# Kernel optimization log

Hardware: AMD Instinct MI355X
Metric: run time of the kernel (lower is better)

The kernel has to match this reference:

```python
import jax, jax.numpy as jnp
import numpy as np
from jax import lax

C = 128       # capacity
D = 64        # latent_dims
K = 512       # K_vecs
BETA = 0.25
DN = ('NCHW', 'OIHW', 'NCHW')


def conv(x, w, b, stride=2, pad=1):
    y = lax.conv_general_dilated(x, w, (stride, stride), ((pad, pad), (pad, pad)),
                                 dimension_numbers=DN)
    return y + b[None, :, None, None]


def conv_transpose(x, w, b, stride=2, pad=1, k=4):
    # PyTorch ConvTranspose2d weight is (Cin, Cout, kh, kw); emulate via
    # lhs-dilated conv with spatially flipped, IO-swapped kernel.
    w2 = jnp.flip(w, axis=(-2, -1)).transpose(1, 0, 2, 3)  # -> OIHW
    p = k - 1 - pad
    y = lax.conv_general_dilated(x, w2, (1, 1), ((p, p), (p, p)),
                                 lhs_dilation=(stride, stride), dimension_numbers=DN)
    return y + b[None, :, None, None]


def setup_inputs() -> dict:
    key = jax.random.key(0)
    ks = jax.random.split(key, 11)
    s = 0.05
    return {
        'x': jax.random.uniform(ks[0], (32, 1, 256, 256), dtype=jnp.float32),
        'enc_w1': jax.random.normal(ks[1], (C, 1, 4, 4), jnp.float32) * s,
        'enc_b1': jnp.zeros((C,), jnp.float32),
        'enc_w2': jax.random.normal(ks[2], (D, C, 4, 4), jnp.float32) * s,
        'enc_b2': jnp.zeros((D,), jnp.float32),
        'codebook': jax.random.normal(ks[3], (K, D), jnp.float32),
        'dec_w2': jax.random.normal(ks[4], (D, C, 4, 4), jnp.float32) * s,  # ConvT: (Cin,Cout,kh,kw)
        'dec_b2': jnp.zeros((C,), jnp.float32),
        'dec_w1': jax.random.normal(ks[5], (C, 1, 4, 4), jnp.float32) * s,
        'dec_b1': jnp.zeros((1,), jnp.float32),
    }


def reference(x, enc_w1, enc_b1, enc_w2, enc_b2, codebook, dec_w2, dec_b2, dec_w1, dec_b1):
    # ---- encoder ----
    h = jax.nn.relu(conv(x, enc_w1, enc_b1))
    z = jax.nn.relu(conv(h, enc_w2, enc_b2))          # [B, D, H/4, W/4]

    # ---- vector quantizer ----
    z_nhwc = jnp.transpose(z, (0, 2, 3, 1))           # [B, h, w, D]
    flat = z_nhwc.reshape(-1, D)                      # [N, D]
    # mean-over-D squared distance, expanded form (no NxKxD tensor)
    d = (jnp.sum(flat * flat, axis=1, keepdims=True)
         - 2.0 * flat @ codebook.T
         + jnp.sum(codebook * codebook, axis=1)[None, :]) / D   # [N, K]
    idx = jnp.argmin(d, axis=1)                       # [N]
    quantized = codebook[idx].reshape(z_nhwc.shape)   # [B, h, w, D]

    codebook_loss = jnp.mean((quantized - lax.stop_gradient(z_nhwc)) ** 2)
    commitment_loss = jnp.mean((lax.stop_gradient(quantized) - z_nhwc) ** 2)
    vq_loss = codebook_loss + BETA * commitment_loss

    # straight-through estimator (training mode)
    quantized_st = z_nhwc + lax.stop_gradient(quantized - z_nhwc)
    q_nchw = jnp.transpose(quantized_st, (0, 3, 1, 2))

    # ---- decoder ----
    g = jax.nn.relu(conv_transpose(q_nchw, dec_w2, dec_b2))
    x_recon = jax.nn.sigmoid(conv_transpose(g, dec_w1, dec_b1))

    return vq_loss, idx[:, None].astype(jnp.int32), x_recon
```

## Files before the change

kernel.cpp:

```cpp
#include <hip/hip_runtime.h>
#include <math.h>


#define REC_OFF 131073

typedef unsigned short ushort_t;
typedef __attribute__((ext_vector_type(8))) short bf16x8;
typedef __attribute__((ext_vector_type(4))) float f32x4;
typedef __attribute__((ext_vector_type(4))) unsigned int u32x4;
union FragU { u32x4 u; bf16x8 h; };

__device__ __forceinline__ unsigned pack_hilo(float v) {
  unsigned u = __float_as_uint(v);
  unsigned htop = u & 0xFFFF0000u;
  float rf = v - __uint_as_float(htop);
  return htop | (__float_as_uint(rf) >> 16);
}

__global__ __launch_bounds__(64) void zero_loss_k(float* __restrict__ out) {
  if (threadIdx.x == 0) out[0] = 0.f;
}

__global__ __launch_bounds__(256) void repackA2_k(
    const float* __restrict__ ew2,
    ushort_t* __restrict__ hi, ushort_t* __restrict__ lo) {
  int idx = blockIdx.x * 256 + threadIdx.x;
  int j = idx & 7, l = (idx >> 3) & 63, mt = (idx >> 9) & 3, ks = idx >> 11;
  int ci = ((ks >> 2) << 3) + ((l >> 4) << 1) + (j >> 2);
  int ky = ks & 3, kx = j & 3, d = (mt << 4) + (l & 15);
  float val = ew2[((d << 7) + ci) * 16 + (ky << 2) + kx];
  unsigned u = __float_as_uint(val);
  float rf = val - __uint_as_float(u & 0xFFFF0000u);
  hi[idx] = (ushort_t)(u >> 16);
  lo[idx] = (ushort_t)(__float_as_uint(rf) >> 16);
}

__global__ __launch_bounds__(256) void repackA_k(
    const float* __restrict__ dw2,
    ushort_t* __restrict__ hi, ushort_t* __restrict__ lo) {
  int idx = blockIdx.x * 256 + threadIdx.x;
  int j = idx & 7, l = (idx >> 3) & 63, mt = (idx >> 9) & 7;
  int s = (idx >> 12) & 7, v = idx >> 15;
  int co = (mt << 4) + (l & 15);
  int ci = (s << 3) + ((l >> 4) << 1) + (j >> 2);
  int tap = j & 3;
  int Yp = v >> 1, pX = v & 1;
  int kyA = 1 - Yp, kyB = kyA + 2;
  int kxA = pX ? 0 : 1, kxB = kxA + 2;
  int ky = (tap & 2) ? kyB : kyA;
  int kx = (tap & 1) ? kxA : kxB;
  float val = dw2[(((ci << 7) + co) << 4) + (ky << 2) + kx];
  unsigned u = __float_as_uint(val);
  float rf = val - __uint_as_float(u & 0xFFFF0000u);
  hi[idx] = (ushort_t)(u >> 16);
  lo[idx] = (ushort_t)(__float_as_uint(rf) >> 16);
}

__global__ __launch_bounds__(256) void repackCB_k(
    const float* __restrict__ cb,
    ushort_t* __restrict__ hi, ushort_t* __restrict__ lo) {
  int idx = blockIdx.x * 256 + threadIdx.x;
  int j = idx & 7, l = (idx >> 3) & 63, mt = (idx >> 9) & 31, ks = idx >> 14;
  int code = (mt << 4) + (l & 15);
  int k = (ks << 5) + ((l >> 4) << 3) + j;
  float val = cb[(code << 6) + k];
  unsigned u = __float_as_uint(val);
  float rf = val - __uint_as_float(u & 0xFFFF0000u);
  hi[idx] = (ushort_t)(u >> 16);
  lo[idx] = (ushort_t)(__float_as_uint(rf) >> 16);
}

__global__ __launch_bounds__(256) void csqF_k(
    const float* __restrict__ cb, float* __restrict__ csqF) {
  int idx = blockIdx.x * 256 + threadIdx.x;
  int r = idx & 3, l = (idx >> 2) & 63, mt = idx >> 8;
  int code = (mt << 4) + ((l >> 4) << 2) + r;
  const float* cp = cb + (code << 6);
  float s = 0.f;
#pragma unroll
  for (int d = 0; d < 64; ++d) s = fmaf(cp[d], cp[d], s);
  csqF[idx] = s;
}

__global__ __launch_bounds__(128) void conv1_k(
    const float* __restrict__ x, const float* __restrict__ w1,
    const float* __restrict__ b1, unsigned* __restrict__ hp) {
  int oy = blockIdx.x, b = blockIdx.y, ox = threadIdx.x;
  float xv[16];
#pragma unroll
  for (int ky = 0; ky < 4; ++ky) {
    int iy = 2 * oy - 1 + ky;
#pragma unroll
    for (int kx = 0; kx < 4; ++kx) {
      int ix = 2 * ox - 1 + kx;
      float v = 0.f;
      if (iy >= 0 && iy < 256 && ix >= 0 && ix < 256)
        v = x[(b * 256 + iy) * 256 + ix];
      xv[ky * 4 + kx] = v;
    }
  }
  for (int c = 0; c < 128; ++c) {
    const float* wp = w1 + c * 16;
    float acc = b1[c];
#pragma unroll
    for (int k = 0; k < 16; ++k) acc = fmaf(xv[k], wp[k], acc);
    hp[((b * 128 + c) * 128 + oy) * 128 + ox] = pack_hilo(fmaxf(acc, 0.f));
  }
}

#define C2RL 133
__global__ __launch_bounds__(256) void conv2_k(
    const unsigned* __restrict__ hp, const ushort_t* __restrict__ wCh,
    const ushort_t* __restrict__ wCl, const float* __restrict__ b2,
    float* __restrict__ z) {
  __shared__ unsigned hs[8][4][C2RL];
  int y = blockIdx.x, b = blockIdx.y;
  int t = threadIdx.x, l = t & 63;
  int w = __builtin_amdgcn_readfirstlane(t >> 6);
  int g = l >> 4;

  if (t < 64) hs[t >> 3][(t >> 1) & 3][(t & 1) ? 129 : 0] = 0u;

  int ci_l = t >> 5, l32 = t & 31;
  int iy[4];
  bool rowok[4];
#pragma unroll
  for (int r = 0; r < 4; ++r) {
    iy[r] = 2 * y - 1 + r;
    rowok[r] = iy[r] >= 0 && iy[r] < 128;
  }
  const unsigned* hbase = hp + (((long)b * 128) << 14);

  u32x4 pre[4];
#pragma unroll
  for (int r = 0; r < 4; ++r)
    pre[r] = rowok[r]
        ? *reinterpret_cast<const u32x4*>(
              hbase + (((long)ci_l << 14) + (iy[r] << 7)) + 4 * l32)
        : (u32x4)0u;

  f32x4 acc[4];
#pragma unroll
  for (int nt = 0; nt < 4; ++nt) acc[nt] = (f32x4)0.f;

  for (int rnd = 0; rnd < 16; ++rnd) {
    __syncthreads();
#pragma unroll
    for (int r = 0; r < 4; ++r) {
      unsigned* dst = &hs[ci_l][r][1 + 4 * l32];
      dst[0] = pre[r][0]; dst[1] = pre[r][1];
      dst[2] = pre[r][2]; dst[3] = pre[r][3];
    }
    __syncthreads();
    if (rnd < 15) {
      long cb8 = ((long)((rnd + 1) * 8 + ci_l)) << 14;
#pragma unroll
      for (int r = 0; r < 4; ++r)
        pre[r] = rowok[r]
            ? *reinterpret_cast<const u32x4*>(
                  hbase + cb8 + (iy[r] << 7) + 4 * l32)
            : (u32x4)0u;
    }
#pragma unroll
    for (int ky = 0; ky < 4; ++ky) {
      int ks = (rnd << 2) + ky;
      FragU ah, al_;
      long aoff = (((long)ks * 4 + w) * 64 + l) * 8;
      ah.u = *reinterpret_cast<const u32x4*>(wCh + aoff);
      al_.u = *reinterpret_cast<const u32x4*>(wCl + aoff);
#pragma unroll
      for (int nt = 0; nt < 4; ++nt) {
        const unsigned* pa = &hs[g * 2][ky][(nt << 5) + 2 * (l & 15)];
        const unsigned* pb = &hs[g * 2 + 1][ky][(nt << 5) + 2 * (l & 15)];
        unsigned a0 = pa[0], a1 = pa[1], a2 = pa[2], a3 = pa[3];
        unsigned b0 = pb[0], b1 = pb[1], b2_ = pb[2], b3 = pb[3];
        FragU bh, bl;
        bh.u[0] = __builtin_amdgcn_perm(a1, a0, 0x07060302u);
        bl.u[0] = __builtin_amdgcn_perm(a1, a0, 0x05040100u);
        bh.u[1] = __builtin_amdgcn_perm(a3, a2, 0x07060302u);
        bl.u[1] = __builtin_amdgcn_perm(a3, a2, 0x05040100u);
        bh.u[2] = __builtin_amdgcn_perm(b1, b0, 0x07060302u);
        bl.u[2] = __builtin_amdgcn_perm(b1, b0, 0x05040100u);
        bh.u[3] = __builtin_amdgcn_perm(b3, b2_, 0x07060302u);
        bl.u[3] = __builtin_amdgcn_perm(b3, b2_, 0x05040100u);
        acc[nt] = __builtin_amdgcn_mfma_f32_16x16x32_bf16(
            ah.h, bh.h, acc[nt], 0, 0, 0);
        acc[nt] = __builtin_amdgcn_mfma_f32_16x16x32_bf16(
            ah.h, bl.h, acc[nt], 0, 0, 0);
        acc[nt] = __builtin_amdgcn_mfma_f32_16x16x32_bf16(
            al_.h, bh.h, acc[nt], 0, 0, 0);
      }
    }
  }
#pragma unroll
  for (int nt = 0; nt < 4; ++nt) {
#pragma unroll
    for (int r = 0; r < 4; ++r) {
      int d = (w << 4) + (g << 2) + r;
      int x = (nt << 4) + (l & 15);
      float v = fmaxf(acc[nt][r] + b2[d], 0.f);
      z[((b * 64 + d) * 64 + y) * 64 + x] = v;
    }
  }
}

__global__ __launch_bounds__(256) void vq_k(
    const float* z, const float* __restrict__ cb,
    const ushort_t* __restrict__ cbFh, const ushort_t* __restrict__ cbFl,
    const float* __restrict__ csqF, unsigned int* q_pk,
    float* __restrict__ out, int n0) {
  __shared__ unsigned zS[64 * 67];
  __shared__ int bk_arr[64];
  __shared__ float redl[4];
  int t = threadIdx.x, l = t & 63;
  int w = __builtin_amdgcn_readfirstlane(t >> 6);
  int nbase = blockIdx.x * 64;
  int b = nbase >> 12, y = (nbase >> 6) & 63;
  long zbase = (long)b * 262144 + y * 64;

  float zv[16];
#pragma unroll
  for (int j = 0; j < 16; ++j) {
    zv[j] = z[zbase + (long)((w << 4) + j) * 4096 + l];
    zS[l * 67 + (w << 4) + j] = pack_hilo(zv[j]);
  }
  __syncthreads();

  int pp = (w << 4) + (l & 15);
  FragU bh[2], bl[2];
#pragma unroll
  for (int ks = 0; ks < 2; ++ks) {
    const unsigned* zp = &zS[pp * 67 + (ks << 5) + ((l >> 4) << 3)];
    unsigned u0 = zp[0], u1 = zp[1], u2 = zp[2], u3 = zp[3];
    unsigned u4 = zp[4], u5 = zp[5], u6 = zp[6], u7 = zp[7];
    bh[ks].u[0] = __builtin_amdgcn_perm(u1, u0, 0x07060302u);
    bl[ks].u[0] = __builtin_amdgcn_perm(u1, u0, 0x05040100u);
    bh[ks].u[1] = __builtin_amdgcn_perm(u3, u2, 0x07060302u);
    bl[ks].u[1] = __builtin_amdgcn_perm(u3, u2, 0x05040100u);
    bh[ks].u[2] = __builtin_amdgcn_perm(u5, u4, 0x07060302u);
    bl[ks].u[2] = __builtin_amdgcn_perm(u5, u4, 0x05040100u);
    bh[ks].u[3] = __builtin_amdgcn_perm(u7, u6, 0x07060302u);
    bl[ks].u[3] = __builtin_amdgcn_perm(u7, u6, 0x05040100u);
  }

  int g = l >> 4;
  float bd = 1e30f;
  int bk = 0;
  for (int mc = 0; mc < 4; ++mc) {
    f32x4 acc[8];
#pragma unroll
    for (int m8 = 0; m8 < 8; ++m8) acc[m8] = (f32x4)0.f;
#pragma unroll
    for (int ks = 0; ks < 2; ++ks) {
#pragma unroll
      for (int m8 = 0; m8 < 8; ++m8) {
        long aoff = (((long)(ks * 32 + mc * 8 + m8) * 64) + l) * 8;
        FragU ah, al_;
        ah.u = *reinterpret_cast<const u32x4*>(cbFh + aoff);
        al_.u = *reinterpret_cast<const u32x4*>(cbFl + aoff);
        acc[m8] = __builtin_amdgcn_mfma_f32_16x16x32_bf16(
            ah.h, bh[ks].h, acc[m8], 0, 0, 0);
        acc[m8] = __builtin_amdgcn_mfma_f32_16x16x32_bf16(
            ah.h, bl[ks].h, acc[m8], 0, 0, 0);
        acc[m8] = __builtin_amdgcn_mfma_f32_16x16x32_bf16(
            al_.h, bh[ks].h, acc[m8], 0, 0, 0);
      }
    }
#pragma unroll
    for (int m8 = 0; m8 < 8; ++m8) {
      int mt = mc * 8 + m8;
      f32x4 cq = *reinterpret_cast<const f32x4*>(csqF + ((mt << 6) + l) * 4);
#pragma unroll
      for (int r = 0; r < 4; ++r) {
        float d = fmaf(-2.f, acc[m8][r], cq[r]);
        if (d < bd) { bd = d; bk = (mt << 4) + (g << 2) + r; }
      }
    }
  }
#pragma unroll
  for (int m = 16; m <= 32; m <<= 1) {
    float d2 = __shfl_xor(bd, m);
    int k2 = __shfl_xor(bk, m);
    if (d2 < bd || (d2 == bd && k2 < bk)) { bd = d2; bk = k2; }
  }
  if (l < 16) {
    bk_arr[(w << 4) + l] = bk;
    out[1 + n0 + nbase + (w << 4) + l] = (float)bk;
  }
  __syncthreads();

  int bkp = bk_arr[l];
  const float* cbest = cb + (bkp << 6) + (w << 4);
  float ls = 0.f;
#pragma unroll
  for (int j = 0; j < 16; ++j) {
    float c = cbest[j];
    q_pk[zbase + (long)((w << 4) + j) * 4096 + l] = pack_hilo(c);
    float df = c - zv[j];
    ls = fmaf(df, df, ls);
  }
#pragma unroll
  for (int m = 32; m; m >>= 1) ls += __shfl_xor(ls, m);
  if (l == 0) redl[w] = ls;
  __syncthreads();
  if (t == 0)
    atomicAdd(out, (redl[0] + redl[1] + redl[2] + redl[3]) * (1.25f / 8388608.f));
}

__global__ __launch_bounds__(256) void dconv2_k(
    const unsigned int* __restrict__ q_pk, const ushort_t* __restrict__ wAh,
    const ushort_t* __restrict__ wAl, const float* __restrict__ db2,
    float* __restrict__ g) {
  __shared__ unsigned int rows[64][2][68];
  int Y = blockIdx.x, b = blockIdx.y;
  int t = threadIdx.x, l = t & 63;
  int w = __builtin_amdgcn_readfirstlane(t >> 6);
  int pX = w & 1, coh = w >> 1;
  int yA = (Y + 1) >> 1, yB = yA - 1;
  int v = ((Y & 1) << 1) | pX;

  for (int s = t; s < 64 * 2 * 68; s += 256) {
    int ci = s / 136, r2 = s - ci * 136;
    int r = r2 / 68, i = r2 - r * 68;
    int yy = r ? yB : yA, ix = i - 1;
    unsigned val = 0u;
    if (i < 66 && yy >= 0 && yy < 64 && ix >= 0 && ix < 64)
      val = q_pk[((b * 64 + ci) * 64 + yy) * 64 + ix];
    rows[ci][r][i] = val;
  }
  __syncthreads();

  f32x4 acc[4][4];
#pragma unroll
  for (int mt = 0; mt < 4; ++mt)
#pragma unroll
    for (int nt = 0; nt < 4; ++nt) acc[mt][nt] = (f32x4)0.f;

  for (int s8 = 0; s8 < 8; ++s8) {
    FragU ah[4], al[4];
#pragma unroll
    for (int mt = 0; mt < 4; ++mt) {
      long off = ((((long)(v * 8 + s8) * 8 + (coh * 4 + mt)) * 64 + l) * 8);
      ah[mt].u = *reinterpret_cast<const u32x4*>(wAh + off);
      al[mt].u = *reinterpret_cast<const u32x4*>(wAl + off);
    }
#pragma unroll
    for (int nt = 0; nt < 4; ++nt) {
      int p = nt * 16 + (l & 15) + pX;
      int cc0 = (s8 << 3) + ((l >> 4) << 1);
      unsigned u0 = rows[cc0][0][p], u1 = rows[cc0][0][p + 1];
      unsigned u2 = rows[cc0][1][p], u3 = rows[cc0][1][p + 1];
      unsigned u4 = rows[cc0 + 1][0][p], u5 = rows[cc0 + 1][0][p + 1];
      unsigned u6 = rows[cc0 + 1][1][p], u7 = rows[cc0 + 1][1][p + 1];
      FragU bh, bl;
      bh.u[0] = (u0 >> 16) | (u1 & 0xFFFF0000u);
      bl.u[0] = (u0 & 0xFFFFu) | (u1 << 16);
      bh.u[1] = (u2 >> 16) | (u3 & 0xFFFF0000u);
      bl.u[1] = (u2 & 0xFFFFu) | (u3 << 16);
      bh.u[2] = (u4 >> 16) | (u5 & 0xFFFF0000u);
      bl.u[2] = (u4 & 0xFFFFu) | (u5 << 16);
      bh.u[3] = (u6 >> 16) | (u7 & 0xFFFF0000u);
      bl.u[3] = (u6 & 0xFFFFu) | (u7 << 16);
#pragma unroll
      for (int mt = 0; mt < 4; ++mt) {
        acc[mt][nt] = __builtin_amdgcn_mfma_f32_16x16x32_bf16(
            ah[mt].h, bh.h, acc[mt][nt], 0, 0, 0);
        acc[mt][nt] = __builtin_amdgcn_mfma_f32_16x16x32_bf16(
            ah[mt].h, bl.h, acc[mt][nt], 0, 0, 0);
        acc[mt][nt] = __builtin_amdgcn_mfma_f32_16x16x32_bf16(
            al[mt].h, bh.h, acc[mt][nt], 0, 0, 0);
      }
    }
  }

#pragma unroll
  for (int mt = 0; mt < 4; ++mt) {
#pragma unroll
    for (int r = 0; r < 4; ++r) {
      int co = ((coh * 4 + mt) << 4) + ((l >> 4) << 2) + r;
      float bias = db2[co];
#pragma unroll
      for (int nt = 0; nt < 4; ++nt) {
        int X = ((nt << 4) + (l & 15)) * 2 + pX;
        float val = fmaxf(acc[mt][nt][r] + bias, 0.f);
        g[((b * 128 + co) * 128 + Y) * 128 + X] = val;
      }
    }
  }
}

__global__ __launch_bounds__(256) void dconv1_k(
    const float* __restrict__ g, const float* __restrict__ wd1,
    const float* __restrict__ db1, float* __restrict__ rec) {
  int a2 = blockIdx.x, b = blockIdx.y;
  int t = threadIdx.x;
  int w = __builtin_amdgcn_readfirstlane(t >> 6);
  int l = t & 63;
  int xh = w >> 1, pX = w & 1;
  int L = xh * 64 + l;
  int kxA = pX ? 0 : 1, kxB = kxA + 2;
  int ixH = L + pX, ixL = L + pX - 1;
  bool okH = ixH < 128, okL = ixL >= 0;
  int yy0 = 2 * a2 - 1;
  bool vy[4];
#pragma unroll
  for (int r = 0; r < 4; ++r) vy[r] = (yy0 + r) >= 0 && (yy0 + r) < 128;

  const float* gb = g + ((long)b * 128) * 16384 + (long)yy0 * 128;
  float acc[4] = {0.f, 0.f, 0.f, 0.f};

  for (int ci = 0; ci < 128; ci += 2) {
    const float* p0 = gb + (long)ci * 16384;
    const float* p1 = p0 + 16384;
    float hi0[4], lo0[4], hi1[4], lo1[4];
#pragma unroll
    for (int r = 0; r < 4; ++r) {
      const float* q0 = p0 + r * 128;
      const float* q1 = p1 + r * 128;
      hi0[r] = (vy[r] && okH) ? q0[ixH] : 0.f;
      lo0[r] = (vy[r] && okL) ? q0[ixL] : 0.f;
      hi1[r] = (vy[r] && okH) ? q1[ixH] : 0.f;
      lo1[r] = (vy[r] && okL) ? q1[ixL] : 0.f;
    }
    const float* wp0 = wd1 + ci * 16;
    const float* wp1 = wp0 + 16;
#pragma unroll
    for (int j = 0; j < 4; ++j) {
      int kyA = (j + 1) & 1, kyB = kyA + 2;
      int rA = ((j + 1) >> 1) + 1;
      float v = acc[j];
      v = fmaf(wp0[kyA * 4 + kxA], hi0[rA], v);
      v = fmaf(wp0[kyA * 4 + kxB], lo0[rA], v);
      v = fmaf(wp0[kyB * 4 + kxA], hi0[rA - 1], v);
      v = fmaf(wp0[kyB * 4 + kxB], lo0[rA - 1], v);
      v = fmaf(wp1[kyA * 4 + kxA], hi1[rA], v);
      v = fmaf(wp1[kyA * 4 + kxB], lo1[rA], v);
      v = fmaf(wp1[kyB * 4 + kxA], hi1[rA - 1], v);
      v = fmaf(wp1[kyB * 4 + kxB], lo1[rA - 1], v);
      acc[j] = v;
    }
  }
  float bb = db1[0];
#pragma unroll
  for (int j = 0; j < 4; ++j) {
    float v = acc[j] + bb;
    v = 1.f / (1.f + __expf(-v));
    rec[((b * 256 + 4 * a2 + j) * 256) + 2 * L + pX] = v;
  }
}

extern "C" void kernel_launch(void* const* d_in, const int* in_sizes, int n_in,
                              void* d_out, int out_size, void* d_ws, size_t ws_size,
                              hipStream_t stream) {
  const float* x      = (const float*)d_in[0];
  const float* enc_w1 = (const float*)d_in[1];
  const float* enc_b1 = (const float*)d_in[2];
  const float* enc_w2 = (const float*)d_in[3];
  const float* enc_b2 = (const float*)d_in[4];
  const float* cb     = (const float*)d_in[5];
  const float* dec_w2 = (const float*)d_in[6];
  const float* dec_b2 = (const float*)d_in[7];
  const float* dec_w1 = (const float*)d_in[8];
  const float* dec_b1 = (const float*)d_in[9];

  float* out = (float*)d_out;
  float* ws  = (float*)d_ws;
  ushort_t* wCh  = (ushort_t*)ws;
  ushort_t* wCl  = (ushort_t*)(ws + 65536);
  ushort_t* wAh  = (ushort_t*)(ws + 131072);
  ushort_t* wAl  = (ushort_t*)(ws + 196608);
  ushort_t* cbFh = (ushort_t*)(ws + 262144);
  ushort_t* cbFl = (ushort_t*)(ws + 278528);
  float* csqF = ws + 294912;
  float* dyn  = ws + 303104;

  const size_t PER_IMG = 2097152 + 262144;
  size_t avail = (ws_size / 4 > 303104 + 64) ? ws_size / 4 - 303104 - 64 : 0;
  int CB = 32;
  while (CB > 1 && (size_t)CB * PER_IMG > avail) CB >>= 1;

  zero_loss_k<<<dim3(1), 64, 0, stream>>>(out);
  repackA2_k<<<dim3(512), 256, 0, stream>>>(enc_w2, wCh, wCl);
  repackA_k<<<dim3(512), 256, 0, stream>>>(dec_w2, wAh, wAl);
  repackCB_k<<<dim3(128), 256, 0, stream>>>(cb, cbFh, cbFl);
  csqF_k<<<dim3(32), 256, 0, stream>>>(cb, csqF);

  for (int b0 = 0; b0 < 32; b0 += CB) {
    unsigned* hp = (unsigned*)dyn;
    float* zq = dyn + (size_t)CB * 2097152;
    conv1_k<<<dim3(128, CB), 128, 0, stream>>>(
        x + (size_t)b0 * 65536, enc_w1, enc_b1, hp);
    conv2_k<<<dim3(64, CB), 256, 0, stream>>>(hp, wCh, wCl, enc_b2, zq);
    vq_k<<<dim3(CB * 64), 256, 0, stream>>>(
        zq, cb, cbFh, cbFl, csqF, (unsigned int*)zq, out, b0 * 4096);
    dconv2_k<<<dim3(128, CB), 256, 0, stream>>>(
        (const unsigned int*)zq, wAh, wAl, dec_b2, (float*)dyn );
    dconv1_k<<<dim3(64, CB), 256, 0, stream>>>(
        (float*)dyn , dec_w1, dec_b1, out + REC_OFF + (size_t)b0 * 65536);
  }
}
```

Baseline: 603.8 us.

## Process two output rows per dconv2 block sharing three staged input rows

The transposed-conv kernel now computes two output rows per block with 512 threads. Both rows share one three-row LDS stage instead of each block loading its own two rows, so the launch has half as many blocks. Input rows are loaded with 16-byte vector loads instead of scalar strided loads, and the halo columns are zeroed separately. This reduces redundant global reads of the quantized latent and the staging index arithmetic, at the cost of larger blocks and more shared memory per block, which may reduce occupancy.

```diff
diff --git a/kernel.cpp b/kernel.cpp
--- a/kernel.cpp
+++ b/kernel.cpp
@@ -307,26 +307,37 @@
     atomicAdd(out, (redl[0] + redl[1] + redl[2] + redl[3]) * (1.25f / 8388608.f));
 }
 
-__global__ __launch_bounds__(256) void dconv2_k(
+__global__ __launch_bounds__(512) void dconv2_k(
     const unsigned int* __restrict__ q_pk, const ushort_t* __restrict__ wAh,
     const ushort_t* __restrict__ wAl, const float* __restrict__ db2,
     float* __restrict__ g) {
-  __shared__ unsigned int rows[64][2][68];
-  int Y = blockIdx.x, b = blockIdx.y;
+  __shared__ unsigned int rows[64][3][68];
+  int a = blockIdx.x, b = blockIdx.y;
   int t = threadIdx.x, l = t & 63;
   int w = __builtin_amdgcn_readfirstlane(t >> 6);
-  int pX = w & 1, coh = w >> 1;
-  int yA = (Y + 1) >> 1, yB = yA - 1;
-  int v = ((Y & 1) << 1) | pX;
-
-  for (int s = t; s < 64 * 2 * 68; s += 256) {
-    int ci = s / 136, r2 = s - ci * 136;
-    int r = r2 / 68, i = r2 - r * 68;
-    int yy = r ? yB : yA, ix = i - 1;
-    unsigned val = 0u;
-    if (i < 66 && yy >= 0 && yy < 64 && ix >= 0 && ix < 64)
-      val = q_pk[((b * 64 + ci) * 64 + yy) * 64 + ix];
-    rows[ci][r][i] = val;
+  int Yloc = w >> 2, pX = w & 1, coh = (w >> 1) & 1;
+  int Y = 2 * a + Yloc;
+  int v = (Yloc << 1) | pX;
+  int rA = Yloc + 1, rB = Yloc;
+
+  if (t < 192) {
+    int ci = t & 63, r = t >> 6;
+    rows[ci][r][0] = 0u;
+    rows[ci][r][65] = 0u;
+  }
+  long qb = (long)b * 262144;
+#pragma unroll
+  for (int r = 0; r < 3; ++r) {
+    int yr = a - 1 + r;
+    bool ok = (yr >= 0) && (yr < 64);
+    for (int s = t; s < 1024; s += 512) {
+      int ci = s >> 4, c4 = s & 15;
+      u32x4 val = ok ? *reinterpret_cast<const u32x4*>(
+                           q_pk + qb + ci * 4096 + yr * 64 + (c4 << 2))
+                     : (u32x4)0u;
+      unsigned* dst = &rows[ci][r][1 + (c4 << 2)];
+      dst[0] = val[0]; dst[1] = val[1]; dst[2] = val[2]; dst[3] = val[3];
+    }
   }
   __syncthreads();
 
@@ -348,10 +359,10 @@
     for (int nt = 0; nt < 4; ++nt) {
       int p = nt * 16 + (l & 15) + pX;
       int cc0 = (s8 << 3) + ((l >> 4) << 1);
-      unsigned u0 = rows[cc0][0][p], u1 = rows[cc0][0][p + 1];
-      unsigned u2 = rows[cc0][1][p], u3 = rows[cc0][1][p + 1];
-      unsigned u4 = rows[cc0 + 1][0][p], u5 = rows[cc0 + 1][0][p + 1];
-      unsigned u6 = rows[cc0 + 1][1][p], u7 = rows[cc0 + 1][1][p + 1];
+      unsigned u0 = rows[cc0][rA][p], u1 = rows[cc0][rA][p + 1];
+      unsigned u2 = rows[cc0][rB][p], u3 = rows[cc0][rB][p + 1];
+      unsigned u4 = rows[cc0 + 1][rA][p], u5 = rows[cc0 + 1][rA][p + 1];
+      unsigned u6 = rows[cc0 + 1][rB][p], u7 = rows[cc0 + 1][rB][p + 1];
       FragU bh, bl;
       bh.u[0] = (u0 >> 16) | (u1 & 0xFFFF0000u);
       bl.u[0] = (u0 & 0xFFFFu) | (u1 << 16);
@@ -493,7 +504,7 @@
     conv2_k<<<dim3(64, CB), 256, 0, stream>>>(hp, wCh, wCl, enc_b2, zq);
     vq_k<<<dim3(CB * 64), 256, 0, stream>>>(
         zq, cb, cbFh, cbFl, csqF, (unsigned int*)zq, out, b0 * 4096);
-    dconv2_k<<<dim3(128, CB), 256, 0, stream>>>(
+    dconv2_k<<<dim3(64, CB), 512, 0, stream>>>(
         (const unsigned int*)zq, wAh, wAl, dec_b2, (float*)dyn );
     dconv1_k<<<dim3(64, CB), 256, 0, stream>>>(
         (float*)dyn , dec_w1, dec_b1, out + REC_OFF + (size_t)b0 * 65536);
```

Result: faster. 561.5 us (-7.0%).
